# Optimization experiments

Measured on AMD Instinct MI355X. Metric: run time of the kernel, lower is better.

The kernel has to match this reference:

```python
import jax, jax.numpy as jnp
import numpy as np

B, P, D = 64, 1024, 768

def setup_inputs() -> dict:
    key = jax.random.key(0)
    k1, k2, k3 = jax.random.split(key, 3)
    z = jax.random.normal(k1, (B, P, D), dtype=jnp.float32)
    q = jax.random.normal(k2, (1, 1, D), dtype=jnp.float32)
    W_proj = jax.random.normal(k3, (D, D), dtype=jnp.float32) * (1.0 / np.sqrt(D))
    return {"z": z, "q": q, "W_proj": W_proj}

def reference(z, q, W_proj):
    # k = Linear(z) with weight W_proj (torch: z @ W.T), no bias
    k = jnp.einsum("bpd,ed->bpe", z, W_proj)          # [B,P,D]
    d = z.shape[-1]
    scale = 1.0 / jnp.sqrt(jnp.asarray(d, dtype=z.dtype))
    # single learnable query broadcast over batch: scores [B,1,P]
    scores = jnp.einsum("xqd,bpd->bqp", q, k) * scale
    attn = jax.nn.softmax(scores, axis=-1)            # [B,1,P]
    pooled = jnp.einsum("bqp,bpd->bqd", attn, z)      # [B,1,D]
    return pooled[:, 0, :]                            # [B,D]
```

## Files before the change

kernel.cpp:

```cpp
#include <hip/hip_runtime.h>
#include <math.h>

#define BB 64
#define PP 1024
#define DD 768

__global__ __launch_bounds__(256) void zero_kernel(float* __restrict__ qw,
                                                   float* __restrict__ out) {
    int i = blockIdx.x * 256 + threadIdx.x;
    if (i < DD) qw[i] = 0.f;
    if (i < BB * DD) out[i] = 0.f;
}

__global__ __launch_bounds__(256) void qw_kernel(const float* __restrict__ q,
                                                 const float* __restrict__ W,
                                                 float* __restrict__ qw) {
    int d  = blockIdx.x * 256 + threadIdx.x;
    int e0 = blockIdx.y * 24;
    float acc = 0.f;
#pragma unroll
    for (int i = 0; i < 24; ++i) {
        int e = e0 + i;
        acc += q[e] * W[(size_t)e * DD + d];
    }
    atomicAdd(&qw[d], acc);
}

__global__ __launch_bounds__(256) void scores_kernel(const float* __restrict__ z,
                                                     const float* __restrict__ qw,
                                                     float* __restrict__ scores) {
    __shared__ float4 qws[DD / 4];
    int tid = threadIdx.x;
    const float4* qw4 = (const float4*)qw;
    if (tid < DD / 4) qws[tid] = qw4[tid];
    __syncthreads();

    int b     = blockIdx.x >> 8;
    int pbase = (blockIdx.x & 255) * 4;
    int wave  = tid >> 6;
    int lane  = tid & 63;
    int p     = pbase + wave;

    const float4* z4 = (const float4*)(z + ((size_t)b * PP + p) * DD);
    float acc = 0.f;
#pragma unroll
    for (int j = 0; j < 3; ++j) {
        float4 zv = z4[lane + 64 * j];
        float4 qv = qws[lane + 64 * j];
        acc += zv.x * qv.x + zv.y * qv.y + zv.z * qv.z + zv.w * qv.w;
    }
#pragma unroll
    for (int off = 32; off >= 1; off >>= 1)
        acc += __shfl_xor(acc, off, 64);

    if (lane == 0)
        scores[b * PP + p] = acc * 0.03608439182435161f;
}

__global__ __launch_bounds__(1024) void softmax_kernel(const float* __restrict__ scores,
                                                       float* __restrict__ attn) {
    int b = blockIdx.x;
    int tid = threadIdx.x;
    int wave = tid >> 6, lane = tid & 63;

    float s = scores[b * PP + tid];

    __shared__ float redm[16];
    float m = s;
#pragma unroll
    for (int off = 32; off >= 1; off >>= 1) m = fmaxf(m, __shfl_xor(m, off, 64));
    if (lane == 0) redm[wave] = m;
    __syncthreads();
    if (wave == 0) {
        float v = (lane < 16) ? redm[lane] : -INFINITY;
#pragma unroll
        for (int off = 8; off >= 1; off >>= 1) v = fmaxf(v, __shfl_xor(v, off, 64));
        if (lane == 0) redm[0] = v;
    }
    __syncthreads();
    m = redm[0];

    float e = __expf(s - m);

    __shared__ float reds[16];
    float t = e;
#pragma unroll
    for (int off = 32; off >= 1; off >>= 1) t += __shfl_xor(t, off, 64);
    if (lane == 0) reds[wave] = t;
    __syncthreads();
    if (wave == 0) {
        float v = (lane < 16) ? reds[lane] : 0.f;
#pragma unroll
        for (int off = 8; off >= 1; off >>= 1) v += __shfl_xor(v, off, 64);
        if (lane == 0) reds[0] = v;
    }
    __syncthreads();

    attn[b * PP + tid] = e / reds[0];
}

__global__ __launch_bounds__(256) void pool_kernel(const float* __restrict__ z,
                                                   const float* __restrict__ attn,
                                                   float* __restrict__ out) {
    int b  = blockIdx.x;
    int dc = blockIdx.y;
    int ps = blockIdx.z;
    int tid = threadIdx.x;
    int d  = dc * 256 + tid;
    int p0 = ps * 128;

    __shared__ float aw[128];
    if (tid < 128) aw[tid] = attn[b * PP + p0 + tid];
    __syncthreads();

    const float* zb = z + ((size_t)b * PP + p0) * DD + d;
    float acc = 0.f;
#pragma unroll 4
    for (int i = 0; i < 128; ++i) acc += aw[i] * zb[(size_t)i * DD];

    atomicAdd(&out[b * DD + d], acc);
}

extern "C" void kernel_launch(void* const* d_in, const int* in_sizes, int n_in,
                              void* d_out, int out_size, void* d_ws, size_t ws_size,
                              hipStream_t stream) {
    const float* z = (const float*)d_in[0];
    const float* q = (const float*)d_in[1];
    const float* W = (const float*)d_in[2];
    float* out = (float*)d_out;

    char* ws = (char*)d_ws;
    float* qw     = (float*)ws;
    float* scores = (float*)(ws + 4096);
    float* attn   = (float*)(ws + 4096 + (size_t)BB * PP * 4);

    zero_kernel<<<(BB * DD + 255) / 256, 256, 0, stream>>>(qw, out);
    dim3 qg(3, 32);
    qw_kernel<<<qg, 256, 0, stream>>>(q, W, qw);
    scores_kernel<<<BB * PP / 4, 256, 0, stream>>>(z, qw, scores);
    softmax_kernel<<<BB, 1024, 0, stream>>>(scores, attn);
    dim3 pg(BB, 3, 8);
    pool_kernel<<<pg, 256, 0, stream>>>(z, attn, out);
}
```

Measured before the change: 305.7 us.

## Fuse scores, softmax and pooling into single-pass online-softmax split kernel

Replaces the separate scores, softmax and pooling kernels with one kernel that reads each row of z once. Each wave keeps a running max, a running sum and a weighted accumulator for 16 rows, and writes its partial result. A second kernel merges the 64 partials per batch with log-sum-exp rescaling, so z is read once instead of twice and the output no longer needs atomics. The trade-offs are a serial dependency chain of exp and rescale work per row and extra workspace traffic for the partials. It also swaps the zeroing kernel for a memset.

```diff
diff --git a/kernel.cpp b/kernel.cpp
--- a/kernel.cpp
+++ b/kernel.cpp
@@ -4,13 +4,8 @@
 #define BB 64
 #define PP 1024
 #define DD 768
-
-__global__ __launch_bounds__(256) void zero_kernel(float* __restrict__ qw,
-                                                   float* __restrict__ out) {
-    int i = blockIdx.x * 256 + threadIdx.x;
-    if (i < DD) qw[i] = 0.f;
-    if (i < BB * DD) out[i] = 0.f;
-}
+#define PS 16
+#define NPART 64
 
 __global__ __launch_bounds__(256) void qw_kernel(const float* __restrict__ q,
                                                  const float* __restrict__ W,
@@ -26,99 +21,93 @@
     atomicAdd(&qw[d], acc);
 }
 
-__global__ __launch_bounds__(256) void scores_kernel(const float* __restrict__ z,
-                                                     const float* __restrict__ qw,
-                                                     float* __restrict__ scores) {
-    __shared__ float4 qws[DD / 4];
-    int tid = threadIdx.x;
+__global__ __launch_bounds__(256) void fused_kernel(const float* __restrict__ z,
+                                                    const float* __restrict__ qw,
+                                                    float* __restrict__ macc,
+                                                    float* __restrict__ ml) {
+    const float scale = 0.03608439182435161f;
+    int b    = blockIdx.x;
+    int ps   = blockIdx.y;
+    int tid  = threadIdx.x;
+    int wave = tid >> 6;
+    int lane = tid & 63;
+
     const float4* qw4 = (const float4*)qw;
-    if (tid < DD / 4) qws[tid] = qw4[tid];
-    __syncthreads();
+    float4 q0 = qw4[lane], q1 = qw4[lane + 64], q2 = qw4[lane + 128];
 
-    int b     = blockIdx.x >> 8;
-    int pbase = (blockIdx.x & 255) * 4;
-    int wave  = tid >> 6;
-    int lane  = tid & 63;
-    int p     = pbase + wave;
+    int p0 = ps * 64 + wave * 16;
+    const float4* zr = (const float4*)(z + ((size_t)b * PP + p0) * DD);
 
-    const float4* z4 = (const float4*)(z + ((size_t)b * PP + p) * DD);
-    float acc = 0.f;
+    float m = -INFINITY, l = 0.f;
+    float4 a0 = {0.f, 0.f, 0.f, 0.f}, a1 = a0, a2 = a0;
+
+    for (int i = 0; i < 16; ++i) {
+        float4 z0 = zr[lane], z1 = zr[lane + 64], z2 = zr[lane + 128];
+        zr += DD / 4;
+
+        float dacc = z0.x * q0.x + z0.y * q0.y + z0.z * q0.z + z0.w * q0.w
+                   + z1.x * q1.x + z1.y * q1.y + z1.z * q1.z + z1.w * q1.w
+                   + z2.x * q2.x + z2.y * q2.y + z2.z * q2.z + z2.w * q2.w;
 #pragma unroll
-    for (int j = 0; j < 3; ++j) {
-        float4 zv = z4[lane + 64 * j];
-        float4 qv = qws[lane + 64 * j];
-        acc += zv.x * qv.x + zv.y * qv.y + zv.z * qv.z + zv.w * qv.w;
+        for (int off = 32; off >= 1; off >>= 1)
+            dacc += __shfl_xor(dacc, off, 64);
+
+        float s  = dacc * scale;
+        float mn = fmaxf(m, s);
+        float alpha = __expf(m - mn);
+        float e     = __expf(s - mn);
+        l = l * alpha + e;
+        a0.x = a0.x * alpha + e * z0.x;  a0.y = a0.y * alpha + e * z0.y;
+        a0.z = a0.z * alpha + e * z0.z;  a0.w = a0.w * alpha + e * z0.w;
+        a1.x = a1.x * alpha + e * z1.x;  a1.y = a1.y * alpha + e * z1.y;
+        a1.z = a1.z * alpha + e * z1.z;  a1.w = a1.w * alpha + e * z1.w;
+        a2.x = a2.x * alpha + e * z2.x;  a2.y = a2.y * alpha + e * z2.y;
+        a2.z = a2.z * alpha + e * z2.z;  a2.w = a2.w * alpha + e * z2.w;
+        m = mn;
     }
-#pragma unroll
-    for (int off = 32; off >= 1; off >>= 1)
-        acc += __shfl_xor(acc, off, 64);
 
-    if (lane == 0)
-        scores[b * PP + p] = acc * 0.03608439182435161f;
+    int part = b * NPART + ps * 4 + wave;
+    float4* ap4 = (float4*)(macc + (size_t)part * DD);
+    ap4[lane] = a0; ap4[lane + 64] = a1; ap4[lane + 128] = a2;
+    if (lane == 0) { ml[part * 2] = m; ml[part * 2 + 1] = l; }
 }
 
-__global__ __launch_bounds__(1024) void softmax_kernel(const float* __restrict__ scores,
-                                                       float* __restrict__ attn) {
-    int b = blockIdx.x;
-    int tid = threadIdx.x;
-    int wave = tid >> 6, lane = tid & 63;
+__global__ __launch_bounds__(256) void reduce_kernel(const float* __restrict__ macc,
+                                                     const float* __restrict__ ml,
+                                                     float* __restrict__ out) {
+    int b    = blockIdx.x;
+    int tid  = threadIdx.x;
+    int wave = tid >> 6;
+    int lane = tid & 63;
 
-    float s = scores[b * PP + tid];
+    __shared__ float wts[NPART];
+    __shared__ float Lsh;
 
-    __shared__ float redm[16];
-    float m = s;
+    if (wave == 0) {
+        float mk = ml[(b * NPART + lane) * 2];
+        float lk = ml[(b * NPART + lane) * 2 + 1];
+        float M = mk;
 #pragma unroll
-    for (int off = 32; off >= 1; off >>= 1) m = fmaxf(m, __shfl_xor(m, off, 64));
-    if (lane == 0) redm[wave] = m;
-    __syncthreads();
-    if (wave == 0) {
-        float v = (lane < 16) ? redm[lane] : -INFINITY;
+        for (int off = 32; off >= 1; off >>= 1) M = fmaxf(M, __shfl_xor(M, off, 64));
+        float w = __expf(mk - M);
+        float L = w * lk;
 #pragma unroll
-        for (int off = 8; off >= 1; off >>= 1) v = fmaxf(v, __shfl_xor(v, off, 64));
-        if (lane == 0) redm[0] = v;
-    }
-    __syncthreads();
-    m = redm[0];
-
-    float e = __expf(s - m);
-
-    __shared__ float reds[16];
-    float t = e;
-#pragma unroll
-    for (int off = 32; off >= 1; off >>= 1) t += __shfl_xor(t, off, 64);
-    if (lane == 0) reds[wave] = t;
-    __syncthreads();
-    if (wave == 0) {
-        float v = (lane < 16) ? reds[lane] : 0.f;
-#pragma unroll
-        for (int off = 8; off >= 1; off >>= 1) v += __shfl_xor(v, off, 64);
-        if (lane == 0) reds[0] = v;
+        for (int off = 32; off >= 1; off >>= 1) L += __shfl_xor(L, off, 64);
+        wts[lane] = w;
+        if (lane == 0) Lsh = L;
     }
     __syncthreads();
 
-    attn[b * PP + tid] = e / reds[0];
-}
-
-__global__ __launch_bounds__(256) void pool_kernel(const float* __restrict__ z,
-                                                   const float* __restrict__ attn,
-                                                   float* __restrict__ out) {
-    int b  = blockIdx.x;
-    int dc = blockIdx.y;
-    int ps = blockIdx.z;
-    int tid = threadIdx.x;
-    int d  = dc * 256 + tid;
-    int p0 = ps * 128;
-
-    __shared__ float aw[128];
-    if (tid < 128) aw[tid] = attn[b * PP + p0 + tid];
-    __syncthreads();
-
-    const float* zb = z + ((size_t)b * PP + p0) * DD + d;
-    float acc = 0.f;
-#pragma unroll 4
-    for (int i = 0; i < 128; ++i) acc += aw[i] * zb[(size_t)i * DD];
-
-    atomicAdd(&out[b * DD + d], acc);
+    float inv = 1.f / Lsh;
+    const float* base = macc + (size_t)b * NPART * DD;
+#pragma unroll
+    for (int c = 0; c < 3; ++c) {
+        int d = c * 256 + tid;
+        float acc = 0.f;
+#pragma unroll 8
+        for (int k = 0; k < NPART; ++k) acc += wts[k] * base[(size_t)k * DD + d];
+        out[b * DD + d] = acc * inv;
+    }
 }
 
 extern "C" void kernel_launch(void* const* d_in, const int* in_sizes, int n_in,
@@ -130,15 +119,14 @@
     float* out = (float*)d_out;
 
     char* ws = (char*)d_ws;
-    float* qw     = (float*)ws;
-    float* scores = (float*)(ws + 4096);
-    float* attn   = (float*)(ws + 4096 + (size_t)BB * PP * 4);
+    float* qw   = (float*)ws;
+    float* ml   = (float*)(ws + 4096);
+    float* macc = (float*)(ws + 4096 + 65536);
 
-    zero_kernel<<<(BB * DD + 255) / 256, 256, 0, stream>>>(qw, out);
+    hipMemsetAsync(qw, 0, DD * sizeof(float), stream);
     dim3 qg(3, 32);
     qw_kernel<<<qg, 256, 0, stream>>>(q, W, qw);
-    scores_kernel<<<BB * PP / 4, 256, 0, stream>>>(z, qw, scores);
-    softmax_kernel<<<BB, 1024, 0, stream>>>(scores, attn);
-    dim3 pg(BB, 3, 8);
-    pool_kernel<<<pg, 256, 0, stream>>>(z, attn, out);
+    dim3 fg(BB, PS);
+    fused_kernel<<<fg, 256, 0, stream>>>(z, qw, macc, ml);
+    reduce_kernel<<<BB, 256, 0, stream>>>(macc, ml, out);
 }
```

Result: faster. 294.7 us (-3.6%).
